# Optimization experiments

Measured on AMD Instinct MI355X. Metric: run time of the kernel, lower is better.

## Reference

```python
import jax, jax.numpy as jnp
import numpy as np

B, L, D_MODEL, N_HEAD, D_K, D_V, VOCAB = 2, 1024, 512, 8, 64, 64, 64
TEMP = float(np.sqrt(D_K))
LN_EPS = 1e-5


def setup_inputs() -> dict:
    key = jax.random.key(0)
    ks = jax.random.split(key, 24)
    inp = {}
    inp['q'] = jax.random.normal(ks[0], (B, L, D_MODEL), jnp.float32)
    inp['k'] = jax.random.normal(ks[1], (B, L, D_MODEL), jnp.float32)
    inp['v'] = jax.random.normal(ks[2], (B, L, D_MODEL), jnp.float32)
    inp['mask'] = jax.random.uniform(ks[3], (B, L, L)) < 0.1
    # tf_f1 carries -1 (padding) positions; its sign defines tf_mask for ALL five features
    inp['tf_f1'] = jax.random.randint(ks[4], (B, L, L), -1, VOCAB, jnp.int32)
    inp['tf_f2'] = jax.random.randint(ks[5], (B, L, L), 0, VOCAB, jnp.int32)
    inp['tf_f3'] = jax.random.randint(ks[6], (B, L, L), 0, VOCAB, jnp.int32)
    inp['tf_f4'] = jax.random.randint(ks[7], (B, L, L), 0, VOCAB, jnp.int32)
    inp['tf_f5'] = jax.random.randint(ks[8], (B, L, L), 0, VOCAB, jnp.int32)
    s_qk = np.sqrt(2.0 / (D_MODEL + D_K))
    s_v = np.sqrt(2.0 / (D_MODEL + D_V))
    inp['w_q'] = jax.random.normal(ks[9], (D_MODEL, N_HEAD * D_K), jnp.float32) * s_qk
    inp['b_q'] = jnp.zeros((N_HEAD * D_K,), jnp.float32)
    inp['w_k'] = jax.random.normal(ks[10], (D_MODEL, N_HEAD * D_K), jnp.float32) * s_qk
    inp['b_k'] = jnp.zeros((N_HEAD * D_K,), jnp.float32)
    inp['w_v'] = jax.random.normal(ks[11], (D_MODEL, N_HEAD * D_V), jnp.float32) * s_v
    inp['b_v'] = jnp.zeros((N_HEAD * D_V,), jnp.float32)
    for i in range(5):
        inp[f'emb{i+1}'] = jax.random.normal(ks[12 + i], (VOCAB, N_HEAD), jnp.float32)
    fc_std = np.sqrt(2.0 / (N_HEAD * D_V + D_MODEL))
    inp['fc_w'] = jax.random.normal(ks[17], (N_HEAD * D_V, D_MODEL), jnp.float32) * fc_std
    inp['fc_b'] = jnp.zeros((D_MODEL,), jnp.float32)
    inp['ln_g'] = jnp.ones((D_MODEL,), jnp.float32)
    inp['ln_b'] = jnp.zeros((D_MODEL,), jnp.float32)
    return inp


def _bias(emb, tf, tf_mask):
    # (tf * mask).long() embedding lookup, zeroed where mask==0 -> [H, B, L, L]
    idx = (tf.astype(jnp.float32) * tf_mask).astype(jnp.int32)
    feat = emb[idx] * tf_mask[..., None]          # [B, L, L, H]
    return jnp.transpose(feat, (3, 0, 1, 2))      # [H, B, L, L]


def reference(q, k, v, mask, tf_f1, tf_f2, tf_f3, tf_f4, tf_f5,
              w_q, b_q, w_k, b_k, w_v, b_v,
              emb1, emb2, emb3, emb4, emb5,
              fc_w, fc_b, ln_g, ln_b):
    residual = q
    qh = (q @ w_q + b_q).reshape(B, L, N_HEAD, D_K)
    kh = (k @ w_k + b_k).reshape(B, L, N_HEAD, D_K)
    vh = (v @ w_v + b_v).reshape(B, L, N_HEAD, D_V)

    scores = jnp.einsum('blhd,bmhd->hblm', qh, kh)  # [H, B, Lq, Lk]
    tf_mask = (tf_f1 >= 0).astype(jnp.float32)      # [B, L, L] (from tf_f1 only, as in torch)
    scores = (scores
              + _bias(emb1, tf_f1, tf_mask)
              + _bias(emb2, tf_f2, tf_mask)
              + _bias(emb3, tf_f3, tf_mask)
              + _bias(emb4, tf_f4, tf_mask)
              + _bias(emb5, tf_f5, tf_mask)) / TEMP
    scores = jnp.where(mask[None], -jnp.inf, scores)
    attn = jax.nn.softmax(scores, axis=-1)          # [H, B, L, L]; dropout = identity (eval)

    out = jnp.einsum('hblm,bmhd->blhd', attn, vh).reshape(B, L, N_HEAD * D_V)
    out = out @ fc_w + fc_b                          # dropout = identity (eval)
    out = out + residual
    mu = jnp.mean(out, axis=-1, keepdims=True)
    var = jnp.mean((out - mu) ** 2, axis=-1, keepdims=True)
    out = (out - mu) * jax.lax.rsqrt(var + LN_EPS) * ln_g + ln_b
    return out, attn.reshape(N_HEAD * B, L, L)
```

## Files before the change

### kernel.cpp

```cpp
#include <hip/hip_runtime.h>
#include <math.h>

#define L_SEQ 1024
#define DMODEL 512
#define NHEAD 8
#define NB 2

typedef __attribute__((ext_vector_type(8))) short bf8;
typedef __attribute__((ext_vector_type(4))) float f4;

__device__ __forceinline__ short f2bf(float f) {
    unsigned u = __float_as_uint(f);
    unsigned r = u + 0x7FFF + ((u >> 16) & 1);
    return (short)(r >> 16);
}

__global__ __launch_bounds__(256) void pack_tf_kernel(
    const int* __restrict__ mask,
    const int* __restrict__ tf1, const int* __restrict__ tf2,
    const int* __restrict__ tf3, const int* __restrict__ tf4,
    const int* __restrict__ tf5, unsigned* __restrict__ pk, int n4)
{
    int i = blockIdx.x * 256 + threadIdx.x;
    if (i >= n4) return;
    const int4 mk = ((const int4*)mask)[i];
    const int4 a1 = ((const int4*)tf1)[i];
    const int4 a2 = ((const int4*)tf2)[i];
    const int4 a3 = ((const int4*)tf3)[i];
    const int4 a4 = ((const int4*)tf4)[i];
    const int4 a5 = ((const int4*)tf5)[i];
    uint4 o;
#define PK(F) ((mk.F ? 0x80000000u : 0u) | ((unsigned)(a1.F + 1) << 24) \
               | ((unsigned)a2.F << 18) | ((unsigned)a3.F << 12)        \
               | ((unsigned)a4.F << 6) | (unsigned)a5.F)
    o.x = PK(x); o.y = PK(y); o.z = PK(z); o.w = PK(w);
#undef PK
    ((uint4*)pk)[i] = o;
}

__global__ __launch_bounds__(256) void transpose_cast_kernel(
    const float* __restrict__ s0, const float* __restrict__ s1,
    const float* __restrict__ s2, const float* __restrict__ s3,
    short* __restrict__ d0, short* __restrict__ d1,
    short* __restrict__ d2, short* __restrict__ d3)
{
    const float* src; short* dst;
    switch (blockIdx.z) {
        case 0: src = s0; dst = d0; break;
        case 1: src = s1; dst = d1; break;
        case 2: src = s2; dst = d2; break;
        default: src = s3; dst = d3; break;
    }
    __shared__ float tile[32][33];
    const int tx = threadIdx.x, ty = threadIdx.y;
    const int x0 = blockIdx.x * 32, y0 = blockIdx.y * 32;
#pragma unroll
    for (int j = 0; j < 32; j += 8)
        tile[ty + j][tx] = src[(size_t)(y0 + ty + j) * 512 + x0 + tx];
    __syncthreads();
#pragma unroll
    for (int j = 0; j < 32; j += 8)
        dst[(size_t)(x0 + ty + j) * 512 + y0 + tx] = f2bf(tile[tx][ty + j]);
}

__global__ __launch_bounds__(128) void proj_gemm_kernel(
    const float* __restrict__ q, const float* __restrict__ k,
    const float* __restrict__ v,
    const short* __restrict__ Wtq, const short* __restrict__ Wtk,
    const short* __restrict__ Wtv,
    const float* __restrict__ b_q, const float* __restrict__ b_k,
    const float* __restrict__ b_v,
    short* __restrict__ qh, short* __restrict__ kh, short* __restrict__ vht)
{
    const int z = blockIdx.z;
    const float* A    = (z == 0) ? q   : (z == 1) ? k   : v;
    const short* Bt   = (z == 0) ? Wtq : (z == 1) ? Wtk : Wtv;
    const float* bias = (z == 0) ? b_q : (z == 1) ? b_k : b_v;

    const int w = threadIdx.x >> 6, lane = threadIdx.x & 63;
    const int lr = lane & 15, lq = lane >> 4;
    const int m_base = blockIdx.y * 32 + w * 16;
    const int n_base = blockIdx.x * 32;

    f4 acc[2];
    const f4 zero = {0.f, 0.f, 0.f, 0.f};
    acc[0] = zero; acc[1] = zero;

    for (int k0 = 0; k0 < 512; k0 += 32) {
        const float* p = A + (size_t)(m_base + lr) * 512 + k0 + lq * 8;
        float4 f0 = *(const float4*)p;
        float4 f1 = *(const float4*)(p + 4);
        bf8 a;
        a[0] = f2bf(f0.x); a[1] = f2bf(f0.y); a[2] = f2bf(f0.z); a[3] = f2bf(f0.w);
        a[4] = f2bf(f1.x); a[5] = f2bf(f1.y); a[6] = f2bf(f1.z); a[7] = f2bf(f1.w);
#pragma unroll
        for (int nf = 0; nf < 2; ++nf) {
            bf8 b = *(const bf8*)(Bt + (size_t)(n_base + nf * 16 + lr) * 512 + k0 + lq * 8);
            acc[nf] = __builtin_amdgcn_mfma_f32_16x16x32_bf16(a, b, acc[nf], 0, 0, 0);
        }
    }

    short* Cnat = (z == 0) ? qh : kh;
#pragma unroll
    for (int nf = 0; nf < 2; ++nf) {
        const int n = n_base + nf * 16 + lr;
        const float bv = bias[n];
        const int mrow = m_base + lq * 4;
#pragma unroll
        for (int r = 0; r < 4; ++r) {
            const float val = acc[nf][r] + bv;
            const int m = mrow + r;
            if (z < 2) {
                Cnat[(size_t)m * 512 + n] = f2bf(val);
            } else {
                const int bb = m >> 10, l = m & 1023;
                vht[((size_t)bb * 512 + n) * 1024 + l] = f2bf(val);
            }
        }
    }
}

__global__ __launch_bounds__(512) void flash_attn_kernel(
    const short* __restrict__ qh, const short* __restrict__ kh,
    const short* __restrict__ vht, const unsigned* __restrict__ pk,
    const float* __restrict__ emb1, const float* __restrict__ emb2,
    const float* __restrict__ emb3, const float* __restrict__ emb4,
    const float* __restrict__ emb5,
    float* __restrict__ attn, short* __restrict__ pv)
{
    const int z = blockIdx.x, h = z >> 1, b = z & 1;
    const int t = threadIdx.x;
    const int wave = t >> 6, lane = t & 63;
    const int wr = wave & 1, wm = wave >> 1;
    const int lr = lane & 15, lq = lane >> 4;
    const int l0 = blockIdx.y * 32 + wr * 16;
    const int mbase = wm * 256;

    __shared__ float embs[5][64];
    __shared__ float red_mx[4][2][16];
    __shared__ float red_sm[4][2][16];
    __shared__ short plds[8][1024];
    __shared__ float ored[4][2][16][64];

    if (t < 320) {
        const float* es[5] = {emb1, emb2, emb3, emb4, emb5};
        embs[t >> 6][t & 63] = es[t >> 6][(t & 63) * NHEAD + h];
    }

    const short* qp = qh + ((size_t)(b * L_SEQ + l0 + lr)) * DMODEL + h * 64 + lq * 8;
    const bf8 aq0 = *(const bf8*)qp;
    const bf8 aq1 = *(const bf8*)(qp + 32);

    const int lrow0 = l0 + lq * 4;
    int tboff[4];
#pragma unroll
    for (int r = 0; r < 4; ++r)
        tboff[r] = (b * L_SEQ + lrow0 + r) * L_SEQ + lr;
    const short* kbp = kh + (size_t)b * L_SEQ * DMODEL + h * 64 + lq * 8;

    __syncthreads();

    const f4 zero = {0.f, 0.f, 0.f, 0.f};

#define COMPUTE_S(m0, sv)                                                     \
    {                                                                         \
        f4 acc[4];                                                            \
        acc[0] = zero; acc[1] = zero; acc[2] = zero; acc[3] = zero;           \
        _Pragma("unroll")                                                     \
        for (int nt = 0; nt < 4; ++nt) {                                      \
            const short* kp = kbp + (size_t)((m0) + nt * 16 + lr) * DMODEL;   \
            bf8 b0 = *(const bf8*)kp;                                         \
            bf8 b1 = *(const bf8*)(kp + 32);                                  \
            acc[nt] = __builtin_amdgcn_mfma_f32_16x16x32_bf16(aq0, b0, acc[nt], 0, 0, 0); \
            acc[nt] = __builtin_amdgcn_mfma_f32_16x16x32_bf16(aq1, b1, acc[nt], 0, 0, 0); \
        }                                                                     \
        _Pragma("unroll")                                                     \
        for (int nt = 0; nt < 4; ++nt) {                                      \
            _Pragma("unroll")                                                 \
            for (int r = 0; r < 4; ++r) {                                     \
                const unsigned u = pk[tboff[r] + (m0) + nt * 16];             \
                float sval;                                                   \
                if (u & 0x80000000u) { sval = -INFINITY; }                    \
                else {                                                        \
                    const int i1m = (u >> 24) & 0x7F;                         \
                    float bs = 0.f;                                           \
                    if (i1m) bs = embs[0][i1m - 1] + embs[1][(u >> 18) & 63]  \
                                + embs[2][(u >> 12) & 63]                     \
                                + embs[3][(u >> 6) & 63] + embs[4][u & 63];   \
                    sval = (acc[nt][r] + bs) * 0.125f;                        \
                }                                                             \
                sv[nt][r] = sval;                                             \
            }                                                                 \
        }                                                                     \
    }

    float mx[4], sm[4];
#pragma unroll
    for (int r = 0; r < 4; ++r) { mx[r] = -INFINITY; sm[r] = 0.f; }

    for (int mt = 0; mt < 4; ++mt) {
        const int m0 = mbase + mt * 64;
        float sv[4][4];
        COMPUTE_S(m0, sv);
        float tmx[4];
#pragma unroll
        for (int r = 0; r < 4; ++r)
            tmx[r] = fmaxf(fmaxf(sv[0][r], sv[1][r]), fmaxf(sv[2][r], sv[3][r]));
#pragma unroll
        for (int r = 0; r < 4; ++r) {
#pragma unroll
            for (int off = 1; off < 16; off <<= 1)
                tmx[r] = fmaxf(tmx[r], __shfl_xor(tmx[r], off));
        }
        float mnew[4], tsum[4];
#pragma unroll
        for (int r = 0; r < 4; ++r) { mnew[r] = fmaxf(mx[r], tmx[r]); tsum[r] = 0.f; }
#pragma unroll
        for (int nt = 0; nt < 4; ++nt)
#pragma unroll
            for (int r = 0; r < 4; ++r)
                tsum[r] += (sv[nt][r] > -INFINITY) ? __expf(sv[nt][r] - mnew[r]) : 0.f;
#pragma unroll
        for (int r = 0; r < 4; ++r) {
#pragma unroll
            for (int off = 1; off < 16; off <<= 1)
                tsum[r] += __shfl_xor(tsum[r], off);
        }
#pragma unroll
        for (int r = 0; r < 4; ++r) {
            const float fac = (mx[r] == -INFINITY) ? 0.f : __expf(mx[r] - mnew[r]);
            sm[r] = sm[r] * fac + tsum[r];
            mx[r] = mnew[r];
        }
    }

    if (lr == 0) {
#pragma unroll
        for (int r = 0; r < 4; ++r) {
            red_mx[wm][wr][lq * 4 + r] = mx[r];
            red_sm[wm][wr][lq * 4 + r] = sm[r];
        }
    }
    __syncthreads();

    float mfin[4], inv[4];
#pragma unroll
    for (int r = 0; r < 4; ++r) {
        const int row = lq * 4 + r;
        const float m0_ = red_mx[0][wr][row], m1_ = red_mx[1][wr][row];
        const float m2_ = red_mx[2][wr][row], m3_ = red_mx[3][wr][row];
        const float mf = fmaxf(fmaxf(m0_, m1_), fmaxf(m2_, m3_));
        float s = 0.f;
        if (m0_ > -INFINITY) s += red_sm[0][wr][row] * __expf(m0_ - mf);
        if (m1_ > -INFINITY) s += red_sm[1][wr][row] * __expf(m1_ - mf);
        if (m2_ > -INFINITY) s += red_sm[2][wr][row] * __expf(m2_ - mf);
        if (m3_ > -INFINITY) s += red_sm[3][wr][row] * __expf(m3_ - mf);
        mfin[r] = mf;
        inv[r] = 1.0f / s;
    }

    f4 oacc[4];
    oacc[0] = zero; oacc[1] = zero; oacc[2] = zero; oacc[3] = zero;
    float* ap = attn + (size_t)z * L_SEQ * L_SEQ;
    short* pbase = &plds[wave][0];

    for (int mt = 0; mt < 4; ++mt) {
        const int m0 = mbase + mt * 64;
        float sv[4][4];
        COMPUTE_S(m0, sv);
#pragma unroll
        for (int nt = 0; nt < 4; ++nt) {
#pragma unroll
            for (int r = 0; r < 4; ++r) {
                const float p = (sv[nt][r] > -INFINITY)
                                    ? __expf(sv[nt][r] - mfin[r]) * inv[r] : 0.f;
                ap[(size_t)(lrow0 + r) * L_SEQ + m0 + nt * 16 + lr] = p;
                const int row = lq * 4 + r, col = nt * 16 + lr;
                const int boff = (row * 128 + col * 2) ^ ((row & 7) << 4);
                *(short*)((char*)pbase + boff) = f2bf(p);
            }
        }
        asm volatile("s_waitcnt lgkmcnt(0)" ::: "memory");
#pragma unroll
        for (int kk = 0; kk < 2; ++kk) {
            const int rb = (lr * 128 + (kk * 32 + lq * 8) * 2) ^ ((lr & 7) << 4);
            const bf8 pa = *(const bf8*)((const char*)pbase + rb);
#pragma unroll
            for (int ntd = 0; ntd < 4; ++ntd) {
                const bf8 bv = *(const bf8*)(vht
                    + ((size_t)b * DMODEL + h * 64 + ntd * 16 + lr) * L_SEQ
                    + m0 + kk * 32 + lq * 8);
                oacc[ntd] = __builtin_amdgcn_mfma_f32_16x16x32_bf16(pa, bv, oacc[ntd], 0, 0, 0);
            }
        }
    }
#undef COMPUTE_S

#pragma unroll
    for (int ntd = 0; ntd < 4; ++ntd)
#pragma unroll
        for (int r = 0; r < 4; ++r)
            ored[wm][wr][lq * 4 + r][ntd * 16 + lr] = oacc[ntd][r];
    __syncthreads();
    if (wm == 0) {
#pragma unroll
        for (int ntd = 0; ntd < 4; ++ntd) {
#pragma unroll
            for (int r = 0; r < 4; ++r) {
                const int row = lq * 4 + r;
                const float s = ored[0][wr][row][ntd * 16 + lr]
                              + ored[1][wr][row][ntd * 16 + lr]
                              + ored[2][wr][row][ntd * 16 + lr]
                              + ored[3][wr][row][ntd * 16 + lr];
                pv[((size_t)(b * L_SEQ) + l0 + row) * 512 + h * 64 + ntd * 16 + lr] = f2bf(s);
            }
        }
    }
}

__global__ __launch_bounds__(128) void fc_gemm_kernel(
    const short* __restrict__ A, const short* __restrict__ Bt,
    const float* __restrict__ bias, float* __restrict__ Cout)
{
    const int w = threadIdx.x >> 6, lane = threadIdx.x & 63;
    const int lr = lane & 15, lq = lane >> 4;
    const int m_base = blockIdx.y * 32 + w * 16;
    const int n_base = blockIdx.x * 32;

    f4 acc[2];
    const f4 zero = {0.f, 0.f, 0.f, 0.f};
    acc[0] = zero; acc[1] = zero;

    for (int k0 = 0; k0 < 512; k0 += 32) {
        bf8 a = *(const bf8*)(A + (size_t)(m_base + lr) * 512 + k0 + lq * 8);
#pragma unroll
        for (int nf = 0; nf < 2; ++nf) {
            bf8 b = *(const bf8*)(Bt + (size_t)(n_base + nf * 16 + lr) * 512 + k0 + lq * 8);
            acc[nf] = __builtin_amdgcn_mfma_f32_16x16x32_bf16(a, b, acc[nf], 0, 0, 0);
        }
    }

#pragma unroll
    for (int nf = 0; nf < 2; ++nf) {
        const int n = n_base + nf * 16 + lr;
        const float bv = bias[n];
        const int mrow = m_base + lq * 4;
#pragma unroll
        for (int r = 0; r < 4; ++r)
            Cout[(size_t)(mrow + r) * 512 + n] = acc[nf][r] + bv;
    }
}

__global__ __launch_bounds__(256) void ln_kernel(
    const float* __restrict__ x, const float* __restrict__ res,
    const float* __restrict__ g, const float* __restrict__ bvec,
    float* __restrict__ out)
{
    const int row = blockIdx.x;
    const int t = threadIdx.x;
    float2 xv = ((const float2*)(x + (size_t)row * DMODEL))[t];
    float2 rv = ((const float2*)(res + (size_t)row * DMODEL))[t];
    const float a = xv.x + rv.x;
    const float c = xv.y + rv.y;
    float s = a + c, sq = a * a + c * c;
#pragma unroll
    for (int off = 32; off; off >>= 1) {
        s  += __shfl_down(s, off);
        sq += __shfl_down(sq, off);
    }
    __shared__ float ssum[4], ssq[4];
    __shared__ float smu, srs;
    const int wid = t >> 6, lane = t & 63;
    if (lane == 0) { ssum[wid] = s; ssq[wid] = sq; }
    __syncthreads();
    if (t == 0) {
        float ts = ssum[0] + ssum[1] + ssum[2] + ssum[3];
        float tq = ssq[0] + ssq[1] + ssq[2] + ssq[3];
        float mu = ts * (1.0f / DMODEL);
        float var = tq * (1.0f / DMODEL) - mu * mu;
        smu = mu;
        srs = rsqrtf(var + 1e-5f);
    }
    __syncthreads();
    const float mu = smu, rs = srs;
    float2 gv = ((const float2*)g)[t];
    float2 bv = ((const float2*)bvec)[t];
    float2 o;
    o.x = (a - mu) * rs * gv.x + bv.x;
    o.y = (c - mu) * rs * gv.y + bv.y;
    ((float2*)(out + (size_t)row * DMODEL))[t] = o;
}

extern "C" void kernel_launch(void* const* d_in, const int* in_sizes, int n_in,
                              void* d_out, int out_size, void* d_ws, size_t ws_size,
                              hipStream_t stream)
{
    const float* q    = (const float*)d_in[0];
    const float* k    = (const float*)d_in[1];
    const float* v    = (const float*)d_in[2];
    const int*   mask = (const int*)d_in[3];
    const int*   tf1  = (const int*)d_in[4];
    const int*   tf2  = (const int*)d_in[5];
    const int*   tf3  = (const int*)d_in[6];
    const int*   tf4  = (const int*)d_in[7];
    const int*   tf5  = (const int*)d_in[8];
    const float* w_q  = (const float*)d_in[9];
    const float* b_q  = (const float*)d_in[10];
    const float* w_k  = (const float*)d_in[11];
    const float* b_k  = (const float*)d_in[12];
    const float* w_v  = (const float*)d_in[13];
    const float* b_v  = (const float*)d_in[14];
    const float* emb1 = (const float*)d_in[15];
    const float* emb2 = (const float*)d_in[16];
    const float* emb3 = (const float*)d_in[17];
    const float* emb4 = (const float*)d_in[18];
    const float* emb5 = (const float*)d_in[19];
    const float* fc_w = (const float*)d_in[20];
    const float* fc_b = (const float*)d_in[21];
    const float* ln_g = (const float*)d_in[22];
    const float* ln_b = (const float*)d_in[23];

    float* out  = (float*)d_out;
    float* attn = out + (size_t)NB * L_SEQ * DMODEL;

    char* wsb = (char*)d_ws;
    unsigned* pk = (unsigned*)(wsb + 0);
    short* Wtq  = (short*)(wsb + (8u << 20));
    short* Wtk  = (short*)(wsb + (8u << 20) + (512u << 10));
    short* Wtv  = (short*)(wsb + (9u << 20));
    short* Wtfc = (short*)(wsb + (9u << 20) + (512u << 10));
    short* qh   = (short*)(wsb + (10u << 20));
    short* kh   = (short*)(wsb + (12u << 20));
    short* vht  = (short*)(wsb + (14u << 20));
    short* pv   = (short*)(wsb + (16u << 20));

    const int npk4 = NB * L_SEQ * L_SEQ / 4;

    pack_tf_kernel<<<npk4 / 256, 256, 0, stream>>>(
        mask, tf1, tf2, tf3, tf4, tf5, pk, npk4);

    transpose_cast_kernel<<<dim3(16, 16, 4), dim3(32, 8), 0, stream>>>(
        w_q, w_k, w_v, fc_w, Wtq, Wtk, Wtv, Wtfc);

    proj_gemm_kernel<<<dim3(16, 64, 3), 128, 0, stream>>>(
        q, k, v, Wtq, Wtk, Wtv, b_q, b_k, b_v, qh, kh, vht);

    flash_attn_kernel<<<dim3(16, 32), 512, 0, stream>>>(
        qh, kh, vht, pk, emb1, emb2, emb3, emb4, emb5, attn, pv);

    fc_gemm_kernel<<<dim3(16, 64), 128, 0, stream>>>(pv, Wtfc, fc_b, out);

    ln_kernel<<<NB * L_SEQ, 256, 0, stream>>>(out, q, ln_g, ln_b, out);
}
```

Measured before the change: 300.7 us.

## Split fused attention into register-resident softmax kernel and separate AV GEMM

Result: faster. 278.1 us (-7.5%).

```diff
diff --git a/kernel.cpp b/kernel.cpp
--- a/kernel.cpp
+++ b/kernel.cpp
@@ -120,31 +120,29 @@
     }
 }
 
-__global__ __launch_bounds__(512) void flash_attn_kernel(
+__global__ __launch_bounds__(256) void ssm_kernel(
     const short* __restrict__ qh, const short* __restrict__ kh,
-    const short* __restrict__ vht, const unsigned* __restrict__ pk,
+    const unsigned* __restrict__ pk,
     const float* __restrict__ emb1, const float* __restrict__ emb2,
     const float* __restrict__ emb3, const float* __restrict__ emb4,
     const float* __restrict__ emb5,
-    float* __restrict__ attn, short* __restrict__ pv)
+    float* __restrict__ attn)
 {
     const int z = blockIdx.x, h = z >> 1, b = z & 1;
     const int t = threadIdx.x;
     const int wave = t >> 6, lane = t & 63;
-    const int wr = wave & 1, wm = wave >> 1;
     const int lr = lane & 15, lq = lane >> 4;
-    const int l0 = blockIdx.y * 32 + wr * 16;
-    const int mbase = wm * 256;
+    const int l0 = blockIdx.y * 16;
+    const int mbase = wave * 256;
 
     __shared__ float embs[5][64];
-    __shared__ float red_mx[4][2][16];
-    __shared__ float red_sm[4][2][16];
-    __shared__ short plds[8][1024];
-    __shared__ float ored[4][2][16][64];
-
-    if (t < 320) {
+    __shared__ float red_mx[4][16];
+    __shared__ float red_sm[4][16];
+
+    {
         const float* es[5] = {emb1, emb2, emb3, emb4, emb5};
-        embs[t >> 6][t & 63] = es[t >> 6][(t & 63) * NHEAD + h];
+        for (int i = t; i < 320; i += 256)
+            embs[i >> 6][i & 63] = es[i >> 6][(i & 63) * NHEAD + h];
     }
 
     const short* qp = qh + ((size_t)(b * L_SEQ + l0 + lr)) * DMODEL + h * 64 + lq * 8;
@@ -162,160 +160,149 @@
 
     const f4 zero = {0.f, 0.f, 0.f, 0.f};
 
-#define COMPUTE_S(m0, sv)                                                     \
-    {                                                                         \
-        f4 acc[4];                                                            \
-        acc[0] = zero; acc[1] = zero; acc[2] = zero; acc[3] = zero;           \
-        _Pragma("unroll")                                                     \
-        for (int nt = 0; nt < 4; ++nt) {                                      \
-            const short* kp = kbp + (size_t)((m0) + nt * 16 + lr) * DMODEL;   \
-            bf8 b0 = *(const bf8*)kp;                                         \
-            bf8 b1 = *(const bf8*)(kp + 32);                                  \
-            acc[nt] = __builtin_amdgcn_mfma_f32_16x16x32_bf16(aq0, b0, acc[nt], 0, 0, 0); \
-            acc[nt] = __builtin_amdgcn_mfma_f32_16x16x32_bf16(aq1, b1, acc[nt], 0, 0, 0); \
-        }                                                                     \
-        _Pragma("unroll")                                                     \
-        for (int nt = 0; nt < 4; ++nt) {                                      \
-            _Pragma("unroll")                                                 \
-            for (int r = 0; r < 4; ++r) {                                     \
-                const unsigned u = pk[tboff[r] + (m0) + nt * 16];             \
-                float sval;                                                   \
-                if (u & 0x80000000u) { sval = -INFINITY; }                    \
-                else {                                                        \
-                    const int i1m = (u >> 24) & 0x7F;                         \
-                    float bs = 0.f;                                           \
-                    if (i1m) bs = embs[0][i1m - 1] + embs[1][(u >> 18) & 63]  \
-                                + embs[2][(u >> 12) & 63]                     \
-                                + embs[3][(u >> 6) & 63] + embs[4][u & 63];   \
-                    sval = (acc[nt][r] + bs) * 0.125f;                        \
-                }                                                             \
-                sv[nt][r] = sval;                                             \
-            }                                                                 \
-        }                                                                     \
-    }
-
-    float mx[4], sm[4];
-#pragma unroll
-    for (int r = 0; r < 4; ++r) { mx[r] = -INFINITY; sm[r] = 0.f; }
-
-    for (int mt = 0; mt < 4; ++mt) {
-        const int m0 = mbase + mt * 64;
-        float sv[4][4];
-        COMPUTE_S(m0, sv);
-        float tmx[4];
-#pragma unroll
-        for (int r = 0; r < 4; ++r)
-            tmx[r] = fmaxf(fmaxf(sv[0][r], sv[1][r]), fmaxf(sv[2][r], sv[3][r]));
+    float sv[16][4];
+#pragma unroll
+    for (int tile = 0; tile < 16; ++tile) {
+        const int m0 = mbase + tile * 16;
+        f4 acc = zero;
+        const short* kp = kbp + (size_t)(m0 + lr) * DMODEL;
+        const bf8 b0 = *(const bf8*)kp;
+        const bf8 b1 = *(const bf8*)(kp + 32);
+        acc = __builtin_amdgcn_mfma_f32_16x16x32_bf16(aq0, b0, acc, 0, 0, 0);
+        acc = __builtin_amdgcn_mfma_f32_16x16x32_bf16(aq1, b1, acc, 0, 0, 0);
 #pragma unroll
         for (int r = 0; r < 4; ++r) {
-#pragma unroll
-            for (int off = 1; off < 16; off <<= 1)
-                tmx[r] = fmaxf(tmx[r], __shfl_xor(tmx[r], off));
-        }
-        float mnew[4], tsum[4];
-#pragma unroll
-        for (int r = 0; r < 4; ++r) { mnew[r] = fmaxf(mx[r], tmx[r]); tsum[r] = 0.f; }
-#pragma unroll
-        for (int nt = 0; nt < 4; ++nt)
-#pragma unroll
-            for (int r = 0; r < 4; ++r)
-                tsum[r] += (sv[nt][r] > -INFINITY) ? __expf(sv[nt][r] - mnew[r]) : 0.f;
-#pragma unroll
-        for (int r = 0; r < 4; ++r) {
-#pragma unroll
-            for (int off = 1; off < 16; off <<= 1)
-                tsum[r] += __shfl_xor(tsum[r], off);
-        }
-#pragma unroll
-        for (int r = 0; r < 4; ++r) {
-            const float fac = (mx[r] == -INFINITY) ? 0.f : __expf(mx[r] - mnew[r]);
-            sm[r] = sm[r] * fac + tsum[r];
-            mx[r] = mnew[r];
-        }
-    }
-
+            const unsigned u = pk[tboff[r] + m0];
+            float sval;
+            if (u & 0x80000000u) { sval = -INFINITY; }
+            else {
+                const int i1m = (u >> 24) & 0x7F;
+                float bs = 0.f;
+                if (i1m) bs = embs[0][i1m - 1] + embs[1][(u >> 18) & 63]
+                            + embs[2][(u >> 12) & 63]
+                            + embs[3][(u >> 6) & 63] + embs[4][u & 63];
+                sval = (acc[r] + bs) * 0.125f;
+            }
+            sv[tile][r] = sval;
+        }
+    }
+
+    float mx[4];
+#pragma unroll
+    for (int r = 0; r < 4; ++r) mx[r] = -INFINITY;
+#pragma unroll
+    for (int tile = 0; tile < 16; ++tile)
+#pragma unroll
+        for (int r = 0; r < 4; ++r) mx[r] = fmaxf(mx[r], sv[tile][r]);
+#pragma unroll
+    for (int r = 0; r < 4; ++r) {
+#pragma unroll
+        for (int off = 1; off < 16; off <<= 1)
+            mx[r] = fmaxf(mx[r], __shfl_xor(mx[r], off));
+    }
     if (lr == 0) {
 #pragma unroll
-        for (int r = 0; r < 4; ++r) {
-            red_mx[wm][wr][lq * 4 + r] = mx[r];
-            red_sm[wm][wr][lq * 4 + r] = sm[r];
-        }
-    }
-    __syncthreads();
-
-    float mfin[4], inv[4];
+        for (int r = 0; r < 4; ++r) red_mx[wave][lq * 4 + r] = mx[r];
+    }
+    __syncthreads();
+
+    float mf[4];
 #pragma unroll
     for (int r = 0; r < 4; ++r) {
         const int row = lq * 4 + r;
-        const float m0_ = red_mx[0][wr][row], m1_ = red_mx[1][wr][row];
-        const float m2_ = red_mx[2][wr][row], m3_ = red_mx[3][wr][row];
-        const float mf = fmaxf(fmaxf(m0_, m1_), fmaxf(m2_, m3_));
-        float s = 0.f;
-        if (m0_ > -INFINITY) s += red_sm[0][wr][row] * __expf(m0_ - mf);
-        if (m1_ > -INFINITY) s += red_sm[1][wr][row] * __expf(m1_ - mf);
-        if (m2_ > -INFINITY) s += red_sm[2][wr][row] * __expf(m2_ - mf);
-        if (m3_ > -INFINITY) s += red_sm[3][wr][row] * __expf(m3_ - mf);
-        mfin[r] = mf;
-        inv[r] = 1.0f / s;
-    }
-
-    f4 oacc[4];
-    oacc[0] = zero; oacc[1] = zero; oacc[2] = zero; oacc[3] = zero;
+        mf[r] = fmaxf(fmaxf(red_mx[0][row], red_mx[1][row]),
+                      fmaxf(red_mx[2][row], red_mx[3][row]));
+    }
+
+    float sm[4] = {0.f, 0.f, 0.f, 0.f};
+#pragma unroll
+    for (int tile = 0; tile < 16; ++tile) {
+#pragma unroll
+        for (int r = 0; r < 4; ++r) {
+            const float e = (sv[tile][r] > -INFINITY) ? __expf(sv[tile][r] - mf[r]) : 0.f;
+            sv[tile][r] = e;
+            sm[r] += e;
+        }
+    }
+#pragma unroll
+    for (int r = 0; r < 4; ++r) {
+#pragma unroll
+        for (int off = 1; off < 16; off <<= 1)
+            sm[r] += __shfl_xor(sm[r], off);
+    }
+    if (lr == 0) {
+#pragma unroll
+        for (int r = 0; r < 4; ++r) red_sm[wave][lq * 4 + r] = sm[r];
+    }
+    __syncthreads();
+
+    float inv[4];
+#pragma unroll
+    for (int r = 0; r < 4; ++r) {
+        const int row = lq * 4 + r;
+        const float s = (red_sm[0][row] + red_sm[1][row])
+                      + (red_sm[2][row] + red_sm[3][row]);
+        inv[r] = (s > 0.f) ? 1.0f / s : 0.f;
+    }
+
     float* ap = attn + (size_t)z * L_SEQ * L_SEQ;
-    short* pbase = &plds[wave][0];
-
-    for (int mt = 0; mt < 4; ++mt) {
-        const int m0 = mbase + mt * 64;
-        float sv[4][4];
-        COMPUTE_S(m0, sv);
+#pragma unroll
+    for (int tile = 0; tile < 16; ++tile) {
+#pragma unroll
+        for (int r = 0; r < 4; ++r)
+            ap[(size_t)(lrow0 + r) * L_SEQ + mbase + tile * 16 + lr] = sv[tile][r] * inv[r];
+    }
+}
+
+__global__ __launch_bounds__(256) void av_mfma_kernel(
+    const float* __restrict__ attn, const short* __restrict__ vht,
+    short* __restrict__ pv)
+{
+    const int z = blockIdx.y, h = z >> 1, b = z & 1;
+    const int w = threadIdx.x >> 6, lane = threadIdx.x & 63;
+    const int lr = lane & 15, lq = lane >> 4;
+    const int l0 = blockIdx.x * 16;
+    const float* Ab = attn + (size_t)z * L_SEQ * L_SEQ;
+    const short* Bb = vht + ((size_t)b * 512 + h * 64) * 1024;
+
+    f4 acc[4];
+    const f4 zero = {0.f, 0.f, 0.f, 0.f};
+#pragma unroll
+    for (int nt = 0; nt < 4; ++nt) acc[nt] = zero;
+
+    const int kbeg = w * 256;
+    for (int k0 = kbeg; k0 < kbeg + 256; k0 += 32) {
+        const float* p = Ab + (size_t)(l0 + lr) * 1024 + k0 + lq * 8;
+        float4 f0 = *(const float4*)p;
+        float4 f1 = *(const float4*)(p + 4);
+        bf8 a;
+        a[0] = f2bf(f0.x); a[1] = f2bf(f0.y); a[2] = f2bf(f0.z); a[3] = f2bf(f0.w);
+        a[4] = f2bf(f1.x); a[5] = f2bf(f1.y); a[6] = f2bf(f1.z); a[7] = f2bf(f1.w);
 #pragma unroll
         for (int nt = 0; nt < 4; ++nt) {
-#pragma unroll
-            for (int r = 0; r < 4; ++r) {
-                const float p = (sv[nt][r] > -INFINITY)
-                                    ? __expf(sv[nt][r] - mfin[r]) * inv[r] : 0.f;
-                ap[(size_t)(lrow0 + r) * L_SEQ + m0 + nt * 16 + lr] = p;
-                const int row = lq * 4 + r, col = nt * 16 + lr;
-                const int boff = (row * 128 + col * 2) ^ ((row & 7) << 4);
-                *(short*)((char*)pbase + boff) = f2bf(p);
-            }
-        }
-        asm volatile("s_waitcnt lgkmcnt(0)" ::: "memory");
-#pragma unroll
-        for (int kk = 0; kk < 2; ++kk) {
-            const int rb = (lr * 128 + (kk * 32 + lq * 8) * 2) ^ ((lr & 7) << 4);
-            const bf8 pa = *(const bf8*)((const char*)pbase + rb);
-#pragma unroll
-            for (int ntd = 0; ntd < 4; ++ntd) {
-                const bf8 bv = *(const bf8*)(vht
-                    + ((size_t)b * DMODEL + h * 64 + ntd * 16 + lr) * L_SEQ
-                    + m0 + kk * 32 + lq * 8);
-                oacc[ntd] = __builtin_amdgcn_mfma_f32_16x16x32_bf16(pa, bv, oacc[ntd], 0, 0, 0);
-            }
-        }
-    }
-#undef COMPUTE_S
-
-#pragma unroll
-    for (int ntd = 0; ntd < 4; ++ntd)
+            bf8 bv = *(const bf8*)(Bb + (size_t)(nt * 16 + lr) * 1024 + k0 + lq * 8);
+            acc[nt] = __builtin_amdgcn_mfma_f32_16x16x32_bf16(a, bv, acc[nt], 0, 0, 0);
+        }
+    }
+
+    __shared__ float red[4][4][16][17];
+#pragma unroll
+    for (int nt = 0; nt < 4; ++nt)
 #pragma unroll
         for (int r = 0; r < 4; ++r)
-            ored[wm][wr][lq * 4 + r][ntd * 16 + lr] = oacc[ntd][r];
-    __syncthreads();
-    if (wm == 0) {
-#pragma unroll
-        for (int ntd = 0; ntd < 4; ++ntd) {
-#pragma unroll
-            for (int r = 0; r < 4; ++r) {
-                const int row = lq * 4 + r;
-                const float s = ored[0][wr][row][ntd * 16 + lr]
-                              + ored[1][wr][row][ntd * 16 + lr]
-                              + ored[2][wr][row][ntd * 16 + lr]
-                              + ored[3][wr][row][ntd * 16 + lr];
-                pv[((size_t)(b * L_SEQ) + l0 + row) * 512 + h * 64 + ntd * 16 + lr] = f2bf(s);
-            }
-        }
-    }
+            red[w][nt][lq * 4 + r][lr] = acc[nt][r];
+    __syncthreads();
+
+    f4 sum = zero;
+#pragma unroll
+    for (int j = 0; j < 4; ++j)
+#pragma unroll
+        for (int r = 0; r < 4; ++r)
+            sum[r] += red[j][w][lq * 4 + r][lr];
+
+#pragma unroll
+    for (int r = 0; r < 4; ++r)
+        pv[(size_t)(b * L_SEQ + l0 + lq * 4 + r) * 512 + h * 64 + w * 16 + lr] = f2bf(sum[r]);
 }
 
 __global__ __launch_bounds__(128) void fc_gemm_kernel(
@@ -445,8 +432,10 @@
     proj_gemm_kernel<<<dim3(16, 64, 3), 128, 0, stream>>>(
         q, k, v, Wtq, Wtk, Wtv, b_q, b_k, b_v, qh, kh, vht);
 
-    flash_attn_kernel<<<dim3(16, 32), 512, 0, stream>>>(
-        qh, kh, vht, pk, emb1, emb2, emb3, emb4, emb5, attn, pv);
+    ssm_kernel<<<dim3(16, 64), 256, 0, stream>>>(
+        qh, kh, pk, emb1, emb2, emb3, emb4, emb5, attn);
+
+    av_mfma_kernel<<<dim3(64, 16), 256, 0, stream>>>(attn, vht, pv);
 
     fc_gemm_kernel<<<dim3(16, 64), 128, 0, stream>>>(pv, Wtfc, fc_b, out);
 
```
